# Kernel tuning notes

Hardware: AMD Instinct MI355X
Metric: run time of the kernel (lower is better)

The kernel has to match this reference:

```python
import jax, jax.numpy as jnp
import numpy as np

B, S, D = 4, 2048, 1024  # batch, seq_len, isize; FFN hidden = isize, gate dim = 2*isize


def setup_inputs() -> dict:
    key = jax.random.key(0)
    ks = jax.random.split(key, 6)
    sc = lambda n: 1.0 / np.sqrt(n)
    return {
        "iQ": jax.random.normal(ks[0], (B, S, D), jnp.float32),
        "iV": jax.random.normal(ks[1], (B, S, D), jnp.float32),
        "W1": jax.random.normal(ks[2], (D, D), jnp.float32) * sc(D),
        "b1": jnp.zeros((D,), jnp.float32),
        "W2": jax.random.normal(ks[3], (D, D), jnp.float32) * sc(D),
        "b2": jnp.zeros((D,), jnp.float32),
        "Wg": jax.random.normal(ks[4], (2 * D, 2 * D), jnp.float32) * sc(2 * D),
        "bg": jnp.zeros((2 * D,), jnp.float32),
    }


def reference(iQ, iV, W1, b1, W2, b2, Wg, bg):
    seql = iV.shape[1]
    # AAN cumulative-average matrix: row i has 1/(i+1) in cols 0..i (lower triangular)
    inv = 1.0 / jnp.arange(1, seql + 1, dtype=iV.dtype)  # [S]
    attn = jnp.tril(jnp.broadcast_to(inv[:, None], (seql, seql)))  # [S, S]
    avg = jnp.einsum('st,btd->bsd', attn, iV)  # [B, S, D]
    # PositionwiseFF with norm_input=False, dropout=0: Linear -> ReLU -> Linear
    h = jax.nn.relu(avg @ W1 + b1)
    ffn = h @ W2 + b2  # [B, S, D]
    # sigmoid gate over concat(iQ, ffn)
    g = jax.nn.sigmoid(jnp.concatenate([iQ, ffn], axis=-1) @ Wg + bg)  # [B, S, 2D]
    d = ffn.shape[-1]
    igate = g[..., :d]
    fgate = g[..., d:]
    return igate * iQ + fgate * ffn
```

## Files before the change

### kernel.cpp

```cpp
#include <hip/hip_runtime.h>
#include <hip/hip_bf16.h>
#include <cstdint>

typedef unsigned short u16;
typedef unsigned int   u32;

typedef __attribute__((ext_vector_type(8))) short short8;
typedef __attribute__((ext_vector_type(4))) float f32x4;

__device__ __forceinline__ float b2f(u16 v) { return __uint_as_float(((u32)v) << 16); }
__device__ __forceinline__ u16 f2b(float f) {
    u32 u = __float_as_uint(f);
    u += 0x7FFFu + ((u >> 16) & 1u);
    return (u16)(u >> 16);
}

#define G2L16(gp, lp) __builtin_amdgcn_global_load_lds(                       \
    (const __attribute__((address_space(1))) void*)(gp),                      \
    (__attribute__((address_space(3))) void*)(lp), 16, 0, 0)

__device__ __forceinline__ void transpose_body(const float* __restrict__ in,
                                               u16* __restrict__ out,
                                               int R, int C, int lb, int tilesX,
                                               float (*tile)[33]) {
    const int bx = (lb % tilesX) * 32;
    const int by = (lb / tilesX) * 32;
    const int tx = threadIdx.x & 31, ty = threadIdx.x >> 5;
    #pragma unroll
    for (int i = 0; i < 32; i += 8)
        tile[ty + i][tx] = in[(size_t)(by + ty + i) * C + (bx + tx)];
    __syncthreads();
    #pragma unroll
    for (int i = 0; i < 32; i += 8)
        out[(size_t)(bx + ty + i) * R + (by + tx)] = f2b(tile[tx][ty + i]);
}

__global__ void prologue_kernel(const float* __restrict__ W1, u16* __restrict__ W1t,
                                const float* __restrict__ W2, u16* __restrict__ W2t,
                                const float* __restrict__ Wg, u16* __restrict__ Wgt,
                                const float* __restrict__ iQ, u16* __restrict__ iQb,
                                const float* __restrict__ iV, float* __restrict__ csum) {
    __shared__ float tile[32][33];
    const int bid = blockIdx.x;
    const int tid = threadIdx.x;
    if (bid < 1024) {
        transpose_body(W1, W1t, 1024, 1024, bid, 32, tile);
    } else if (bid < 2048) {
        transpose_body(W2, W2t, 1024, 1024, bid - 1024, 32, tile);
    } else if (bid < 6144) {
        transpose_body(Wg, Wgt, 2048, 2048, bid - 2048, 64, tile);
    } else if (bid < 14336) {
        const size_t i = ((size_t)(bid - 6144) * 256 + tid) * 4;
        const float4 v = *(const float4*)(iQ + i);
        ushort4 o;
        o.x = f2b(v.x); o.y = f2b(v.y); o.z = f2b(v.z); o.w = f2b(v.w);
        *(ushort4*)(iQb + i) = o;
    } else {
        const int idx = bid - 14336;
        const int b = idx >> 6, c = idx & 63;
        const int d = tid * 4;
        const float* src = iV + ((size_t)(b * 2048 + c * 32)) * 1024 + d;
        float4 s = {0.f, 0.f, 0.f, 0.f};
        #pragma unroll 8
        for (int i = 0; i < 32; ++i) {
            const float4 v = *(const float4*)(src + (size_t)i * 1024);
            s.x += v.x; s.y += v.y; s.z += v.z; s.w += v.w;
        }
        *(float4*)(csum + ((size_t)(b * 64 + c)) * 1024 + d) = s;
    }
}

__global__ void scan_kernel(const float* __restrict__ iV, const float* __restrict__ csum,
                            u16* __restrict__ avg) {
    const int c = blockIdx.x & 63, b = blockIdx.x >> 6;
    const int d = threadIdx.x * 4;
    const float* cs = csum + (size_t)b * 64 * 1024 + d;
    float4 a0 = {0,0,0,0}, a1 = {0,0,0,0}, a2 = {0,0,0,0}, a3 = {0,0,0,0};
    int cc = 0;
    for (; cc + 4 <= c; cc += 4) {
        const float4 v0 = *(const float4*)(cs + (size_t)(cc + 0) * 1024);
        const float4 v1 = *(const float4*)(cs + (size_t)(cc + 1) * 1024);
        const float4 v2 = *(const float4*)(cs + (size_t)(cc + 2) * 1024);
        const float4 v3 = *(const float4*)(cs + (size_t)(cc + 3) * 1024);
        a0.x += v0.x; a0.y += v0.y; a0.z += v0.z; a0.w += v0.w;
        a1.x += v1.x; a1.y += v1.y; a1.z += v1.z; a1.w += v1.w;
        a2.x += v2.x; a2.y += v2.y; a2.z += v2.z; a2.w += v2.w;
        a3.x += v3.x; a3.y += v3.y; a3.z += v3.z; a3.w += v3.w;
    }
    for (; cc < c; ++cc) {
        const float4 v = *(const float4*)(cs + (size_t)cc * 1024);
        a0.x += v.x; a0.y += v.y; a0.z += v.z; a0.w += v.w;
    }
    float4 acc;
    acc.x = (a0.x + a1.x) + (a2.x + a3.x);
    acc.y = (a0.y + a1.y) + (a2.y + a3.y);
    acc.z = (a0.z + a1.z) + (a2.z + a3.z);
    acc.w = (a0.w + a1.w) + (a2.w + a3.w);

    const size_t off = ((size_t)(b * 2048 + c * 32)) * 1024 + d;
    const float* src = iV + off;
    u16*         dst = avg + off;
    const int s0 = c * 32;
    #pragma unroll 4
    for (int i = 0; i < 32; ++i) {
        const float4 v = *(const float4*)(src + (size_t)i * 1024);
        acc.x += v.x; acc.y += v.y; acc.z += v.z; acc.w += v.w;
        const float inv = 1.0f / (float)(s0 + i + 1);
        ushort4 o;
        o.x = f2b(acc.x * inv); o.y = f2b(acc.y * inv);
        o.z = f2b(acc.z * inv); o.w = f2b(acc.w * inv);
        *(ushort4*)(dst + (size_t)i * 1024) = o;
    }
}

template <int EPI>
__global__ __launch_bounds__(256, 2)
void gemm_kernel(const u16* __restrict__ A, const u16* __restrict__ Bt,
                 const float* __restrict__ bias, u16* __restrict__ C,
                 int M, int N, int K) {
    __shared__ u16 As[128 * 64];
    __shared__ u16 Bs[128 * 64];

    const int tid  = threadIdx.x;
    const int m0   = blockIdx.x * 128;
    const int n0   = blockIdx.y * 128;
    const int wave = tid >> 6, lane = tid & 63;
    const int wm   = (wave & 1) << 6;
    const int wn   = (wave >> 1) << 6;
    const int quad = lane >> 4, l16 = lane & 15;

    f32x4 acc[4][4];
    #pragma unroll
    for (int i = 0; i < 4; ++i)
        #pragma unroll
        for (int j = 0; j < 4; ++j) acc[i][j] = (f32x4){0.f, 0.f, 0.f, 0.f};

    int oo[4], rr[4], qq[4];
    #pragma unroll
    for (int j = 0; j < 4; ++j) {
        oo[j] = tid * 16 + j * 4096;
        rr[j] = oo[j] >> 7;
        qq[j] = ((oo[j] >> 4) & 7) ^ (rr[j] & 7);
    }

    const int ktiles = K >> 6;
    for (int kt = 0; kt < ktiles; ++kt) {
        const int kb = kt << 6;
        #pragma unroll
        for (int j = 0; j < 4; ++j) {
            G2L16((const char*)A  + ((size_t)(m0 + rr[j]) * K + kb) * 2 + qq[j] * 16,
                  (char*)As + oo[j]);
            G2L16((const char*)Bt + ((size_t)(n0 + rr[j]) * K + kb) * 2 + qq[j] * 16,
                  (char*)Bs + oo[j]);
        }
        __syncthreads();

        #pragma unroll
        for (int h = 0; h < 2; ++h) {
            short8 af[4], bf[4];
            #pragma unroll
            for (int mi = 0; mi < 4; ++mi) {
                const int R = wm + mi * 16 + l16;
                af[mi] = *(const short8*)(As + R * 64 + ((((h << 2) | quad) ^ (R & 7)) << 3));
            }
            #pragma unroll
            for (int ni = 0; ni < 4; ++ni) {
                const int R = wn + ni * 16 + l16;
                bf[ni] = *(const short8*)(Bs + R * 64 + ((((h << 2) | quad) ^ (R & 7)) << 3));
            }
            #pragma unroll
            for (int mi = 0; mi < 4; ++mi)
                #pragma unroll
                for (int ni = 0; ni < 4; ++ni)
                    acc[mi][ni] = __builtin_amdgcn_mfma_f32_16x16x32_bf16(
                        af[mi], bf[ni], acc[mi][ni], 0, 0, 0);
        }
        __syncthreads();
    }

    #pragma unroll
    for (int ni = 0; ni < 4; ++ni) {
        const int col = n0 + wn + ni * 16 + l16;
        const float bv = bias[col];
        #pragma unroll
        for (int mi = 0; mi < 4; ++mi) {
            const int row0 = m0 + wm + mi * 16 + quad * 4;
            #pragma unroll
            for (int r = 0; r < 4; ++r) {
                float v = acc[mi][ni][r] + bv;
                if (EPI == 0) v = fmaxf(v, 0.f);
                C[(size_t)(row0 + r) * N + col] = f2b(v);
            }
        }
    }
}

#define VM4  asm volatile("s_waitcnt vmcnt(4)" ::: "memory")
#define VM0  asm volatile("s_waitcnt vmcnt(0)" ::: "memory")
#define NOVM ((void)0)

#define SA(BUF, MH, T) do {                                                     \
    const char* b_ = ((T) < 16) ? ((const char*)iQb + (size_t)(T) * 128)        \
                                : ((const char*)ffn + (size_t)((T) - 16) * 128); \
    G2L16(b_ + gA[MH][0], (char*)&As[BUF][MH][0] + lo[0]);                      \
    G2L16(b_ + gA[MH][1], (char*)&As[BUF][MH][0] + lo[1]);                      \
  } while (0)

#define SB(BUF, GG, T) do {                                                     \
    const char* b_ = (const char*)Wgt + (size_t)(T) * 128;                      \
    G2L16(b_ + gB[GG][0], (char*)&Bs[BUF][GG][0] + lo[0]);                      \
    G2L16(b_ + gB[GG][1], (char*)&Bs[BUF][GG][0] + lo[1]);                      \
  } while (0)

#define PHASE(BUF, MH, RDB, STAGES, VMW) do {                                   \
    short8 af[4][2];                                                            \
    {                                                                           \
      const char* Ab_ = (const char*)&As[BUF][MH][0];                           \
      _Pragma("unroll")                                                         \
      for (int mi = 0; mi < 4; ++mi) {                                          \
        af[mi][0] = *(const short8*)(Ab_ + aF[mi][0]);                          \
        af[mi][1] = *(const short8*)(Ab_ + aF[mi][1]);                          \
      }                                                                         \
      if (RDB) {                                                                \
        const char* B0_ = (const char*)&Bs[BUF][0][0];                          \
        const char* B1_ = (const char*)&Bs[BUF][1][0];                          \
        _Pragma("unroll")                                                       \
        for (int ni = 0; ni < 2; ++ni) {                                        \
          _Pragma("unroll")                                                     \
          for (int ks = 0; ks < 2; ++ks) {                                      \
            bf[0][ni][ks] = *(const short8*)(B0_ + bF[ni][ks]);                 \
            bf[1][ni][ks] = *(const short8*)(B1_ + bF[ni][ks]);                 \
          }                                                                     \
        }                                                                       \
      }                                                                         \
    }                                                                           \
    STAGES                                                                      \
    __builtin_amdgcn_sched_barrier(0);                                          \
    __builtin_amdgcn_s_barrier();                                               \
    asm volatile("s_waitcnt lgkmcnt(0)" ::: "memory");                          \
    __builtin_amdgcn_sched_barrier(0);                                          \
    __builtin_amdgcn_s_setprio(1);                                              \
    _Pragma("unroll")                                                           \
    for (int ks = 0; ks < 2; ++ks) {                                            \
      _Pragma("unroll")                                                         \
      for (int mi = 0; mi < 4; ++mi) {                                          \
        _Pragma("unroll")                                                       \
        for (int ni = 0; ni < 2; ++ni) {                                        \
          acc[0][(MH) * 4 + mi][ni] = __builtin_amdgcn_mfma_f32_16x16x32_bf16(  \
              af[mi][ks], bf[0][ni][ks], acc[0][(MH) * 4 + mi][ni], 0, 0, 0);   \
          acc[1][(MH) * 4 + mi][ni] = __builtin_amdgcn_mfma_f32_16x16x32_bf16(  \
              af[mi][ks], bf[1][ni][ks], acc[1][(MH) * 4 + mi][ni], 0, 0, 0);   \
        }                                                                       \
      }                                                                         \
    }                                                                           \
    __builtin_amdgcn_s_setprio(0);                                              \
    __builtin_amdgcn_sched_barrier(0);                                          \
    VMW;                                                                        \
    __builtin_amdgcn_s_barrier();                                               \
    __builtin_amdgcn_sched_barrier(0);                                          \
  } while (0)

__global__ __launch_bounds__(512, 2)
void gate4_kernel(const u16* __restrict__ iQb, const u16* __restrict__ ffn,
                  const u16* __restrict__ Wgt, const float* __restrict__ bg,
                  const float* __restrict__ iQ, float* __restrict__ out) {
    __shared__ u16 As[2][2][128 * 64];
    __shared__ u16 Bs[2][2][128 * 64];

    const int tid  = threadIdx.x;
    const int bid  = blockIdx.x;
    const int m0   = (bid & 31) * 256;
    const int n0   = (bid >> 5) * 128;
    const int wave = tid >> 6, lane = tid & 63;
    const int wm   = wave & 1;
    const int wn   = wave >> 1;
    const int quad = lane >> 4, l16 = lane & 15;

    u32 lo[2], gA[2][2], gB[2][2];
    #pragma unroll
    for (int j = 0; j < 2; ++j) {
        const u32 o = (u32)tid * 16 + (u32)j * 8192;
        const u32 r = o >> 7;
        const u32 q = ((o >> 4) & 7) ^ (r & 7);
        lo[j]    = o;
        gA[0][j] = (u32)(m0 + r) * 2048 + q * 16;
        gA[1][j] = (u32)(m0 + 128 + r) * 2048 + q * 16;
        gB[0][j] = (u32)(n0 + r) * 4096 + q * 16;
        gB[1][j] = (u32)(n0 + 1024 + r) * 4096 + q * 16;
    }

    u32 aF[4][2], bF[2][2];
    #pragma unroll
    for (int mi = 0; mi < 4; ++mi) {
        const int R = wm * 64 + mi * 16 + l16;
        #pragma unroll
        for (int ks = 0; ks < 2; ++ks)
            aF[mi][ks] = (u32)R * 128 + (u32)((((ks << 2) | quad) ^ (R & 7)) << 4);
    }
    #pragma unroll
    for (int ni = 0; ni < 2; ++ni) {
        const int R = wn * 32 + ni * 16 + l16;
        #pragma unroll
        for (int ks = 0; ks < 2; ++ks)
            bF[ni][ks] = (u32)R * 128 + (u32)((((ks << 2) | quad) ^ (R & 7)) << 4);
    }

    f32x4 acc[2][8][2];
    #pragma unroll
    for (int g = 0; g < 2; ++g)
        #pragma unroll
        for (int mf = 0; mf < 8; ++mf)
            #pragma unroll
            for (int ni = 0; ni < 2; ++ni)
                acc[g][mf][ni] = (f32x4){0.f, 0.f, 0.f, 0.f};

    short8 bf[2][2][2];

    SA(0, 0, 0); SA(0, 1, 0); SB(0, 0, 0); SB(0, 1, 0);
    SA(1, 0, 1); SB(1, 0, 1);
    VM4;
    __builtin_amdgcn_s_barrier();
    __builtin_amdgcn_sched_barrier(0);

    for (int i = 0; i < 15; ++i) {
        const int t0 = 2 * i, t1 = t0 + 1;
        PHASE(0, 0, 1, SA(1, 1, t1);     SB(1, 1, t1);     , NOVM);
        PHASE(0, 1, 0, SA(0, 0, t0 + 2); SB(0, 0, t0 + 2); , VM4);
        PHASE(1, 0, 1, SB(0, 1, t0 + 2); SA(0, 1, t0 + 2); , NOVM);
        PHASE(1, 1, 0, SA(1, 0, t1 + 2); SB(1, 0, t1 + 2); , VM4);
    }
    PHASE(0, 0, 1, SA(1, 1, 31); SB(1, 1, 31); , NOVM);
    PHASE(0, 1, 0,                             , VM0);
    PHASE(1, 0, 1,                             , NOVM);
    PHASE(1, 1, 0,                             , NOVM);

    #pragma unroll
    for (int ni = 0; ni < 2; ++ni) {
        const int col = n0 + wn * 32 + ni * 16 + l16;
        const float bgi = bg[col];
        const float bgf = bg[col + 1024];
        #pragma unroll
        for (int mh = 0; mh < 2; ++mh)
            #pragma unroll
            for (int mi = 0; mi < 4; ++mi) {
                const int row0 = m0 + mh * 128 + wm * 64 + mi * 16 + quad * 4;
                #pragma unroll
                for (int r = 0; r < 4; ++r) {
                    const size_t idx = (size_t)(row0 + r) * 1024 + col;
                    const float gi = 1.0f / (1.0f + __expf(-(acc[0][mh * 4 + mi][ni][r] + bgi)));
                    const float gf = 1.0f / (1.0f + __expf(-(acc[1][mh * 4 + mi][ni][r] + bgf)));
                    out[idx] = gi * iQ[idx] + gf * b2f(ffn[idx]);
                }
            }
    }
}

extern "C" void kernel_launch(void* const* d_in, const int* in_sizes, int n_in,
                              void* d_out, int out_size, void* d_ws, size_t ws_size,
                              hipStream_t stream) {
    const int B = 4, S = 2048, D = 1024, D2 = 2048;
    const int M = B * S;

    const float* iQ = (const float*)d_in[0];
    const float* iV = (const float*)d_in[1];
    const float* W1 = (const float*)d_in[2];
    const float* b1 = (const float*)d_in[3];
    const float* W2 = (const float*)d_in[4];
    const float* b2 = (const float*)d_in[5];
    const float* Wg = (const float*)d_in[6];
    const float* bg = (const float*)d_in[7];
    float* out = (float*)d_out;

    u16*   regA = (u16*)d_ws;
    u16*   regB = regA + (size_t)M * D;
    u16*   iQb  = regB + (size_t)M * D;
    u16*   W1t  = iQb  + (size_t)M * D;
    u16*   W2t  = W1t  + (size_t)D * D;
    u16*   Wgt  = W2t  + (size_t)D * D;
    float* csum = (float*)(Wgt + (size_t)D2 * D2);

    u16* avg = regA;
    u16* ffn = regA;
    u16* h   = regB;

    prologue_kernel<<<14592, 256, 0, stream>>>(W1, W1t, W2, W2t, Wg, Wgt,
                                               iQ, iQb, iV, csum);
    scan_kernel<<<B * 64, 256, 0, stream>>>(iV, csum, avg);
    gemm_kernel<0><<<dim3(M / 128, D / 128), 256, 0, stream>>>(avg, W1t, b1, h, M, D, D);
    gemm_kernel<1><<<dim3(M / 128, D / 128), 256, 0, stream>>>(h, W2t, b2, ffn, M, D, D);
    gate4_kernel<<<256, 512, 0, stream>>>(iQb, ffn, Wgt, bg, iQ, out);
}
```

Measured before the change: 276.5 us.

## Split gate GEMM phases into eight half-K phases with finer prefetch

Each of the four pipeline phases in the gate GEMM is split into two half-K sub-phases. Each sub-phase reads only one k-slice of A and B fragments from LDS, and the global-to-LDS prefetches are spread across more phases with a deeper vmcnt(6) wait. The aim is to lower register pressure and interleave LDS reads, memory loads and MFMA work more finely. The cost is twice as many barriers per K tile, which may offset the gain.

```diff
diff --git a/kernel.cpp b/kernel.cpp
--- a/kernel.cpp
+++ b/kernel.cpp
@@ -195,7 +195,7 @@
     }
 }
 
-#define VM4  asm volatile("s_waitcnt vmcnt(4)" ::: "memory")
+#define VM6  asm volatile("s_waitcnt vmcnt(6)" ::: "memory")
 #define VM0  asm volatile("s_waitcnt vmcnt(0)" ::: "memory")
 #define NOVM ((void)0)
 
@@ -212,25 +212,20 @@
     G2L16(b_ + gB[GG][1], (char*)&Bs[BUF][GG][0] + lo[1]);                      \
   } while (0)
 
-#define PHASE(BUF, MH, RDB, STAGES, VMW) do {                                   \
-    short8 af[4][2];                                                            \
+#define PHASE(BUF, MH, KS, RDB, STAGES, VMW) do {                               \
+    short8 af[4];                                                               \
     {                                                                           \
       const char* Ab_ = (const char*)&As[BUF][MH][0];                           \
       _Pragma("unroll")                                                         \
-      for (int mi = 0; mi < 4; ++mi) {                                          \
-        af[mi][0] = *(const short8*)(Ab_ + aF[mi][0]);                          \
-        af[mi][1] = *(const short8*)(Ab_ + aF[mi][1]);                          \
-      }                                                                         \
+      for (int mi = 0; mi < 4; ++mi)                                            \
+        af[mi] = *(const short8*)(Ab_ + aF[mi][KS]);                            \
       if (RDB) {                                                                \
         const char* B0_ = (const char*)&Bs[BUF][0][0];                          \
         const char* B1_ = (const char*)&Bs[BUF][1][0];                          \
         _Pragma("unroll")                                                       \
         for (int ni = 0; ni < 2; ++ni) {                                        \
-          _Pragma("unroll")                                                     \
-          for (int ks = 0; ks < 2; ++ks) {                                      \
-            bf[0][ni][ks] = *(const short8*)(B0_ + bF[ni][ks]);                 \
-            bf[1][ni][ks] = *(const short8*)(B1_ + bF[ni][ks]);                 \
-          }                                                                     \
+          bf[0][ni][KS] = *(const short8*)(B0_ + bF[ni][KS]);                   \
+          bf[1][ni][KS] = *(const short8*)(B1_ + bF[ni][KS]);                   \
         }                                                                       \
       }                                                                         \
     }                                                                           \
@@ -241,16 +236,13 @@
     __builtin_amdgcn_sched_barrier(0);                                          \
     __builtin_amdgcn_s_setprio(1);                                              \
     _Pragma("unroll")                                                           \
-    for (int ks = 0; ks < 2; ++ks) {                                            \
+    for (int mi = 0; mi < 4; ++mi) {                                            \
       _Pragma("unroll")                                                         \
-      for (int mi = 0; mi < 4; ++mi) {                                          \
-        _Pragma("unroll")                                                       \
-        for (int ni = 0; ni < 2; ++ni) {                                        \
-          acc[0][(MH) * 4 + mi][ni] = __builtin_amdgcn_mfma_f32_16x16x32_bf16(  \
-              af[mi][ks], bf[0][ni][ks], acc[0][(MH) * 4 + mi][ni], 0, 0, 0);   \
-          acc[1][(MH) * 4 + mi][ni] = __builtin_amdgcn_mfma_f32_16x16x32_bf16(  \
-              af[mi][ks], bf[1][ni][ks], acc[1][(MH) * 4 + mi][ni], 0, 0, 0);   \
-        }                                                                       \
+      for (int ni = 0; ni < 2; ++ni) {                                          \
+        acc[0][(MH) * 4 + mi][ni] = __builtin_amdgcn_mfma_f32_16x16x32_bf16(    \
+            af[mi], bf[0][ni][KS], acc[0][(MH) * 4 + mi][ni], 0, 0, 0);         \
+        acc[1][(MH) * 4 + mi][ni] = __builtin_amdgcn_mfma_f32_16x16x32_bf16(    \
+            af[mi], bf[1][ni][KS], acc[1][(MH) * 4 + mi][ni], 0, 0, 0);         \
       }                                                                         \
     }                                                                           \
     __builtin_amdgcn_s_setprio(0);                                              \
@@ -261,9 +253,9 @@
   } while (0)
 
 __global__ __launch_bounds__(512, 2)
-void gate4_kernel(const u16* __restrict__ iQb, const u16* __restrict__ ffn,
-                  const u16* __restrict__ Wgt, const float* __restrict__ bg,
-                  const float* __restrict__ iQ, float* __restrict__ out) {
+void gate8f_kernel(const u16* __restrict__ iQb, const u16* __restrict__ ffn,
+                   const u16* __restrict__ Wgt, const float* __restrict__ bg,
+                   const float* __restrict__ iQ, float* __restrict__ out) {
     __shared__ u16 As[2][2][128 * 64];
     __shared__ u16 Bs[2][2][128 * 64];
 
@@ -317,22 +309,30 @@
     short8 bf[2][2][2];
 
     SA(0, 0, 0); SA(0, 1, 0); SB(0, 0, 0); SB(0, 1, 0);
-    SA(1, 0, 1); SB(1, 0, 1);
-    VM4;
+    SA(1, 0, 1); SB(1, 0, 1); SB(1, 1, 1);
+    VM6;
     __builtin_amdgcn_s_barrier();
     __builtin_amdgcn_sched_barrier(0);
 
     for (int i = 0; i < 15; ++i) {
         const int t0 = 2 * i, t1 = t0 + 1;
-        PHASE(0, 0, 1, SA(1, 1, t1);     SB(1, 1, t1);     , NOVM);
-        PHASE(0, 1, 0, SA(0, 0, t0 + 2); SB(0, 0, t0 + 2); , VM4);
-        PHASE(1, 0, 1, SB(0, 1, t0 + 2); SA(0, 1, t0 + 2); , NOVM);
-        PHASE(1, 1, 0, SA(1, 0, t1 + 2); SB(1, 0, t1 + 2); , VM4);
-    }
-    PHASE(0, 0, 1, SA(1, 1, 31); SB(1, 1, 31); , NOVM);
-    PHASE(0, 1, 0,                             , VM0);
-    PHASE(1, 0, 1,                             , NOVM);
-    PHASE(1, 1, 0,                             , NOVM);
+        PHASE(0, 0, 0, 1, SA(1, 1, t1);                    , NOVM);
+        PHASE(0, 0, 1, 1,                                  , NOVM);
+        PHASE(0, 1, 0, 0, SA(0, 0, t0 + 2); SB(0, 0, t0 + 2); , NOVM);
+        PHASE(0, 1, 1, 0, SB(0, 1, t0 + 2);                , VM6);
+        PHASE(1, 0, 0, 1, SA(0, 1, t0 + 2);                , NOVM);
+        PHASE(1, 0, 1, 1,                                  , NOVM);
+        PHASE(1, 1, 0, 0, SA(1, 0, t1 + 2); SB(1, 0, t1 + 2); , NOVM);
+        PHASE(1, 1, 1, 0, SB(1, 1, t1 + 2);                , VM6);
+    }
+    PHASE(0, 0, 0, 1, SA(1, 1, 31);                        , NOVM);
+    PHASE(0, 0, 1, 1,                                      , NOVM);
+    PHASE(0, 1, 0, 0,                                      , NOVM);
+    PHASE(0, 1, 1, 0,                                      , VM0);
+    PHASE(1, 0, 0, 1,                                      , NOVM);
+    PHASE(1, 0, 1, 1,                                      , NOVM);
+    PHASE(1, 1, 0, 0,                                      , NOVM);
+    PHASE(1, 1, 1, 0,                                      , NOVM);
 
     #pragma unroll
     for (int ni = 0; ni < 2; ++ni) {
@@ -388,5 +388,5 @@
     scan_kernel<<<B * 64, 256, 0, stream>>>(iV, csum, avg);
     gemm_kernel<0><<<dim3(M / 128, D / 128), 256, 0, stream>>>(avg, W1t, b1, h, M, D, D);
     gemm_kernel<1><<<dim3(M / 128, D / 128), 256, 0, stream>>>(h, W2t, b2, ffn, M, D, D);
-    gate4_kernel<<<256, 512, 0, stream>>>(iQb, ffn, Wgt, bg, iQ, out);
-}
+    gate8f_kernel<<<256, 512, 0, stream>>>(iQb, ffn, Wgt, bg, iQ, out);
+}
```

After: 274.9 us. Within noise of the previous version (-0.6%).
